# Kernel optimization log

Measured on AMD Instinct MI355X. Metric: run time of the kernel, lower is better.

Reference implementation:

```python
import jax, jax.numpy as jnp
import numpy as np

# ---- Cl(3,0) Cayley table, basis order [1, e1, e2, e3, e12, e13, e23, e123] ----
def _build_cayley():
    order = [0b000, 0b001, 0b010, 0b100, 0b011, 0b101, 0b110, 0b111]
    idx = {m: i for i, m in enumerate(order)}
    M = np.zeros((8, 8, 8), np.float32)
    for i, a in enumerate(order):
        for j, b in enumerate(order):
            aa, swaps = a >> 1, 0
            while aa:
                swaps += bin(aa & b).count('1')
                aa >>= 1
            M[i, j, idx[a ^ b]] = -1.0 if (swaps % 2) else 1.0
    return M

CAYLEY = jnp.asarray(_build_cayley())  # (8,8,8): c_k = a_i b_j M[i,j,k]

B, D, H, R, K = 16384, 512, 256, 95, 8

def _layernorm(x, g, b, eps=1e-5):
    mu = jnp.mean(x, axis=-1, keepdims=True)
    var = jnp.var(x, axis=-1, keepdims=True)
    return (x - mu) * jax.lax.rsqrt(var + eps) * g + b

def _proj(h, W1, b1, lg, lb, W2, b2):
    x = h @ W1 + b1
    x = _layernorm(x, lg, lb)
    x = jax.nn.gelu(x, approximate=False)  # torch nn.GELU default = exact erf
    return (x @ W2 + b2).reshape(h.shape[0], K, 8)  # dropout is eval-mode identity

def setup_inputs() -> dict:
    key = jax.random.key(0)
    ks = jax.random.split(key, 16)
    s1, s2 = 1.0 / np.sqrt(D), 1.0 / np.sqrt(H)
    inp = {
        'h_perp': jax.random.normal(ks[0], (B, D), jnp.float32),
        'h_vuln': jax.random.normal(ks[1], (B, D), jnp.float32),
        'Wp1': jax.random.normal(ks[2], (D, H), jnp.float32) * s1,
        'bp1': jnp.zeros((H,), jnp.float32),
        'lgp': jnp.ones((H,), jnp.float32),
        'lbp': jnp.zeros((H,), jnp.float32),
        'Wp2': jax.random.normal(ks[3], (H, K * 8), jnp.float32) * s2,
        'bp2': jnp.zeros((K * 8,), jnp.float32),
        'Wv1': jax.random.normal(ks[4], (D, H), jnp.float32) * s1,
        'bv1': jnp.zeros((H,), jnp.float32),
        'lgv': jnp.ones((H,), jnp.float32),
        'lbv': jnp.zeros((H,), jnp.float32),
        'Wv2': jax.random.normal(ks[5], (H, K * 8), jnp.float32) * s2,
        'bv2': jnp.zeros((K * 8,), jnp.float32),
        'T': jax.random.normal(ks[6], (R, K, 8), jnp.float32) * 0.1,
        'gw': jnp.zeros((8,), jnp.float32).at[0].set(1.0),
    }
    return inp

def reference(h_perp, h_vuln, Wp1, bp1, lgp, lbp, Wp2, bp2,
              Wv1, bv1, lgv, lbv, Wv2, bv2, T, gw):
    m_perp = _proj(h_perp, Wp1, bp1, lgp, lbp, Wp2, bp2)  # (B,K,8)
    m_vuln = _proj(h_vuln, Wv1, bv1, lgv, lbv, Wv2, bv2)  # (B,K,8)
    # triple product: (m_perp x T_r) x m_vuln  via Cayley tensor
    at = jnp.einsum('bki,rkj,ijm->brkm', m_perp, T, CAYLEY)          # (B,R,K,8)
    res = jnp.einsum('brkm,bkj,mjn->brkn', at, m_vuln, CAYLEY)       # (B,R,K,8)
    weighted = jnp.einsum('brkn,n->brk', res, gw)                    # grade-weighted readout
    return jnp.mean(weighted, axis=-1)                               # (B,R) logits
```

## Files before the change

kernel.cpp:

```cpp
#include <hip/hip_runtime.h>
#include <math.h>


#define B_ 16384
#define D_ 512
#define H_ 256
#define R_ 95

typedef __attribute__((ext_vector_type(8))) short short8;
typedef __attribute__((ext_vector_type(4))) float f32x4;

#define MFMA(a, b, c) __builtin_amdgcn_mfma_f32_16x16x32_bf16(a, b, c, 0, 0, 0)

__device__ __forceinline__ short f2bf(float x) {
    union { float f; unsigned u; } v; v.f = x;
    unsigned r = v.u + 0x7fffu + ((v.u >> 16) & 1u);
    return (short)(r >> 16);
}
__device__ __forceinline__ float bf2f(short s) {
    union { float f; unsigned u; } v;
    v.u = ((unsigned)(unsigned short)s) << 16;
    return v.f;
}

__device__ __forceinline__ float gelu_fast(float x) {
    const float z  = x * 0.70710678118654752f;
    const float az = fabsf(z);
    const float t  = 1.0f / fmaf(0.3275911f, az, 1.0f);
    float p = fmaf(1.061405429f, t, -1.453152027f);
    p = fmaf(p, t, 1.421413741f);
    p = fmaf(p, t, -0.284496736f);
    p = fmaf(p, t, 0.254829592f);
    p *= t;
    const float e  = 1.0f - p * __expf(-az * az);
    const float er = copysignf(e, z);
    return 0.5f * x * (1.0f + er);
}

__global__ __launch_bounds__(256)
void cdd_prep_kernel(const float* __restrict__ Wp1, const float* __restrict__ Wv1,
                     const float* __restrict__ Wp2, const float* __restrict__ Wv2,
                     short* __restrict__ W1c_p, short* __restrict__ W1c_v,
                     short* __restrict__ W2t_p, short* __restrict__ W2t_v)
{
    const int o = blockIdx.x * 256 + threadIdx.x;
    if (o < 16 * 256 * 32) {
        const int n = o & 255, kin = (o >> 8) & 31, ch = o >> 13;
        const int src = (ch * 32 + kin) * 256 + n;
        const int dst = ch * 8192 + n * 32 + kin;
        W1c_p[dst] = f2bf(Wp1[src]);
        W1c_v[dst] = f2bf(Wv1[src]);
    }
    if (o < 64 * 256) {
        const int n = o >> 8, k = o & 255;
        W2t_p[o] = f2bf(Wp2[k * 64 + n]);
        W2t_v[o] = f2bf(Wv2[k * 64 + n]);
    }
}

#define PROJ_BODY(Kk, BUF_C, BUF_R, S_I0, S_I1, S_C0, S_C1, WB_USE, WB_LD)  \
  do {                                                                      \
    const int g = gb + (Kk);                                                \
    if (g <= 14) {                         \
      short8 pk;                                                            \
      pk[0]=f2bf(S_C0.x); pk[1]=f2bf(S_C0.y); pk[2]=f2bf(S_C0.z); pk[3]=f2bf(S_C0.w); \
      pk[4]=f2bf(S_C1.x); pk[5]=f2bf(S_C1.y); pk[6]=f2bf(S_C1.z); pk[7]=f2bf(S_C1.w); \
      *(short8*)(hs + (BUF_C) * 2048 + wdst) = pk;                          \
    }                                                                       \
    asm volatile("s_waitcnt lgkmcnt(0)" ::: "memory");  \
    __builtin_amdgcn_s_barrier();                                           \
    asm volatile("" ::: "memory");                                          \
    if (g <= 14) {                            \
      _Pragma("unroll")                                                     \
      for (int nt = 0; nt < 4; ++nt)                                        \
        WB_LD[nt] = *(const short8*)(Wb0 + (g + 1) * 8192 + nt * 512);      \
    }                                                                       \
    {                                                  \
      const short8 a0 = *(const short8*)(hs + (BUF_R) * 2048 + (0 * 64 + l) * 8); \
      const short8 a1 = *(const short8*)(hs + (BUF_R) * 2048 + (1 * 64 + l) * 8); \
      const short8 a2 = *(const short8*)(hs + (BUF_R) * 2048 + (2 * 64 + l) * 8); \
      const short8 a3 = *(const short8*)(hs + (BUF_R) * 2048 + (3 * 64 + l) * 8); \
      _Pragma("unroll")                                                     \
      for (int nt = 0; nt < 4; ++nt) {                                      \
        acc1[0][nt] = MFMA(a0, WB_USE[nt], acc1[0][nt]);                    \
        acc1[1][nt] = MFMA(a1, WB_USE[nt], acc1[1][nt]);                    \
        acc1[2][nt] = MFMA(a2, WB_USE[nt], acc1[2][nt]);                    \
        acc1[3][nt] = MFMA(a3, WB_USE[nt], acc1[3][nt]);                    \
      }                                                                     \
    }                                                                       \
    asm volatile("" ::: "memory");         \
    if (g <= 11) {                       \
      S_I0 = *(const float4*)(hbase + (g + 4) * 32);                        \
      S_I1 = *(const float4*)(hbase + (g + 4) * 32 + 4);                    \
    }                                                                       \
  } while (0)

__global__ __launch_bounds__(256, 2)
void cdd_proj_kernel(const float* __restrict__ h_p, const float* __restrict__ h_v,
                     const float* __restrict__ bp1, const float* __restrict__ lgp,
                     const float* __restrict__ lbp, const float* __restrict__ bp2,
                     const float* __restrict__ bv1, const float* __restrict__ lgv,
                     const float* __restrict__ lbv, const float* __restrict__ bv2,
                     const short* __restrict__ W1c_p, const short* __restrict__ W1c_v,
                     const short* __restrict__ W2t_p, const short* __restrict__ W2t_v,
                     short* __restrict__ mp_out, short* __restrict__ mv_out)
{
    __shared__ __align__(16) short hs[4 * 2048];
    __shared__ __align__(16) short xs[64 * 264];
    __shared__ __align__(16) float lnbuf[512];

    const int which = blockIdx.y;
    const float* __restrict__ h   = which ? h_v : h_p;
    const float* __restrict__ b1  = which ? bv1 : bp1;
    const float* __restrict__ lg  = which ? lgv : lgp;
    const float* __restrict__ lb  = which ? lbv : lbp;
    const float* __restrict__ b2  = which ? bv2 : bp2;
    const short* __restrict__ W1c = which ? W1c_v : W1c_p;
    const short* __restrict__ W2t = which ? W2t_v : W2t_p;
    short* __restrict__ mo = which ? mv_out : mp_out;

    const int t = threadIdx.x;
    const int w = t >> 6, l = t & 63, q = l >> 4, c = l & 15;
    const int b0 = blockIdx.x * 64;
    const int srow = t >> 2, kq4 = (t & 3);
    const int mt_s = srow >> 4, c_s = srow & 15;
    const int wdst = (mt_s * 64 + kq4 * 16 + c_s) * 8;

    f32x4 acc1[4][4];
#pragma unroll
    for (int mt = 0; mt < 4; ++mt)
#pragma unroll
        for (int nt = 0; nt < 4; ++nt) acc1[mt][nt] = 0;

    const short* Wb0 = W1c + (w * 64 + c) * 32 + q * 8;
    const float* hbase = h + (size_t)(b0 + srow) * D_ + kq4 * 8;

    float4 s0a = *(const float4*)(hbase + 0 * 32), s0b = *(const float4*)(hbase + 0 * 32 + 4);
    float4 s1a = *(const float4*)(hbase + 1 * 32), s1b = *(const float4*)(hbase + 1 * 32 + 4);
    float4 s2a = *(const float4*)(hbase + 2 * 32), s2b = *(const float4*)(hbase + 2 * 32 + 4);
    float4 s3a = *(const float4*)(hbase + 3 * 32), s3b = *(const float4*)(hbase + 3 * 32 + 4);
    short8 wbA[4], wbB[4];
#pragma unroll
    for (int nt = 0; nt < 4; ++nt) wbA[nt] = *(const short8*)(Wb0 + nt * 512);
    {
        short8 pk;
        pk[0]=f2bf(s0a.x); pk[1]=f2bf(s0a.y); pk[2]=f2bf(s0a.z); pk[3]=f2bf(s0a.w);
        pk[4]=f2bf(s0b.x); pk[5]=f2bf(s0b.y); pk[6]=f2bf(s0b.z); pk[7]=f2bf(s0b.w);
        *(short8*)(hs + 0 * 2048 + wdst) = pk;
    }

    for (int gb = 0; gb < 16; gb += 4) {
        PROJ_BODY(0, 1, 0, s0a, s0b, s1a, s1b, wbA, wbB);
        PROJ_BODY(1, 2, 1, s1a, s1b, s2a, s2b, wbB, wbA);
        PROJ_BODY(2, 3, 2, s2a, s2b, s3a, s3b, wbA, wbB);
        PROJ_BODY(3, 0, 3, s3a, s3b, s0a, s0b, wbB, wbA);
    }

    float bb[4], gg[4], ee[4];
#pragma unroll
    for (int nt = 0; nt < 4; ++nt) {
        const int col = w * 64 + nt * 16 + c;
        bb[nt] = b1[col]; gg[nt] = lg[col]; ee[nt] = lb[col];
    }
#pragma unroll
    for (int mt = 0; mt < 4; ++mt)
#pragma unroll
        for (int reg = 0; reg < 4; ++reg) {
            float s1 = 0.f, s2 = 0.f;
#pragma unroll
            for (int nt = 0; nt < 4; ++nt) {
                const float a = acc1[mt][nt][reg] + bb[nt];
                acc1[mt][nt][reg] = a;
                s1 += a; s2 += a * a;
            }
#pragma unroll
            for (int m = 1; m <= 8; m <<= 1) {
                s1 += __shfl_xor(s1, m, 64);
                s2 += __shfl_xor(s2, m, 64);
            }
            if (c == 0) {
                const int row = mt * 16 + q * 4 + reg;
                *(float2*)(lnbuf + (w * 64 + row) * 2) = make_float2(s1, s2);
            }
        }
    __syncthreads();
#pragma unroll
    for (int mt = 0; mt < 4; ++mt)
#pragma unroll
        for (int reg = 0; reg < 4; ++reg) {
            const int row = mt * 16 + q * 4 + reg;
            float S1 = 0.f, S2 = 0.f;
#pragma unroll
            for (int w2 = 0; w2 < 4; ++w2) {
                const float2 p = *(const float2*)(lnbuf + (w2 * 64 + row) * 2);
                S1 += p.x; S2 += p.y;
            }
            const float mu  = S1 * (1.f / 256.f);
            const float var = S2 * (1.f / 256.f) - mu * mu;
            const float rs  = rsqrtf(var + 1e-5f);
#pragma unroll
            for (int nt = 0; nt < 4; ++nt) {
                const int col = w * 64 + nt * 16 + c;
                const float xv = (acc1[mt][nt][reg] - mu) * rs * gg[nt] + ee[nt];
                xs[row * 264 + col] = f2bf(gelu_fast(xv));
            }
        }
    __syncthreads();

    f32x4 acc2[4];
#pragma unroll
    for (int mt = 0; mt < 4; ++mt) acc2[mt] = 0;
    const short* W2b = W2t + (w * 16 + c) * 256 + q * 8;
#pragma unroll
    for (int ks = 0; ks < 8; ++ks) {
        const short8 wbk = *(const short8*)(W2b + ks * 32);
#pragma unroll
        for (int mt = 0; mt < 4; ++mt) {
            const short8 xa = *(const short8*)(xs + (mt * 16 + c) * 264 + ks * 32 + q * 8);
            acc2[mt] = MFMA(xa, wbk, acc2[mt]);
        }
    }
    const float bc = b2[w * 16 + c];
#pragma unroll
    for (int mt = 0; mt < 4; ++mt)
#pragma unroll
        for (int reg = 0; reg < 4; ++reg) {
            const int row = mt * 16 + q * 4 + reg;
            mo[(size_t)(b0 + row) * 64 + w * 16 + c] = f2bf(acc2[mt][reg] + bc);
        }
}

__global__ __launch_bounds__(256, 2)
void cdd_cliff_kernel(const short* __restrict__ mp, const short* __restrict__ mv,
                      const float* __restrict__ T, const float* __restrict__ gw,
                      float* __restrict__ out)
{
    __shared__ __align__(16) float wfl[32 * 68];
    __shared__ __align__(16) float ts[95 * 68];
    const int t  = threadIdx.x;
    const int b0 = blockIdx.x * 32;

#pragma unroll
    for (int k = 0; k < 6; ++k) {
        const int o = t + k * 256;
        if (o < 95 * 16) {
            const int rr = o >> 4, c4 = (o & 15) << 2;
            *(float4*)(ts + rr * 68 + c4) = *(const float4*)(T + rr * 64 + c4);
        }
    }

    {
        const int row = t >> 3, kq = t & 7;
        float g[8];
#pragma unroll
        for (int i = 0; i < 8; ++i) g[i] = gw[i];
        const short8 p8 = *(const short8*)(mp + (size_t)(b0 + row) * 64 + kq * 8);
        const short8 q8 = *(const short8*)(mv + (size_t)(b0 + row) * 64 + kq * 8);
        float mpv[8], mvv[8];
#pragma unroll
        for (int i = 0; i < 8; ++i) { mpv[i] = bf2f(p8[i]); mvv[i] = bf2f(q8[i]); }

        constexpr int MSK[8] = {0, 1, 2, 4, 3, 5, 6, 7};
        float v[8];
#pragma unroll
        for (int m = 0; m < 8; ++m) {
            float s = 0.f;
#pragma unroll
            for (int j = 0; j < 8; ++j) {
                const int am = MSK[m], bm = MSK[j];
                const int par = (__popc((am >> 1) & bm) + __popc((am >> 2) & bm)) & 1;
                const float sg = par ? -1.f : 1.f;
                s = fmaf(sg * g[MSK[am ^ bm]], mvv[j], s);
            }
            v[m] = s;
        }
#pragma unroll
        for (int l2 = 0; l2 < 8; ++l2) {
            float s = 0.f;
#pragma unroll
            for (int i = 0; i < 8; ++i) {
                const int am = MSK[i], bm = MSK[l2];
                const int par = (__popc((am >> 1) & bm) + __popc((am >> 2) & bm)) & 1;
                const float sg = par ? -1.f : 1.f;
                s = fmaf(sg * mpv[i], v[MSK[am ^ bm]], s);
            }
            wfl[row * 68 + kq * 8 + l2] = s;
        }
    }
    __syncthreads();

    {
        const int rr = t >> 3, rl = t & 7;
        float4 wv[16];
#pragma unroll
        for (int cc = 0; cc < 16; ++cc)
            wv[cc] = *(const float4*)(wfl + rr * 68 + cc * 4);
#pragma unroll
        for (int k = 0; k < 12; ++k) {
            const int r = rl + (k << 3);
            if (r < R_) {
                float s = 0.f;
#pragma unroll
                for (int cc = 0; cc < 16; ++cc) {
                    const float4 tv = *(const float4*)(ts + r * 68 + cc * 4);
                    s += wv[cc].x * tv.x + wv[cc].y * tv.y
                       + wv[cc].z * tv.z + wv[cc].w * tv.w;
                }
                out[(size_t)(b0 + rr) * R_ + r] = 0.125f * s;
            }
        }
    }
}

extern "C" void kernel_launch(void* const* d_in, const int* in_sizes, int n_in,
                              void* d_out, int out_size, void* d_ws, size_t ws_size,
                              hipStream_t stream)
{
    const float* h_p = (const float*)d_in[0];
    const float* h_v = (const float*)d_in[1];
    const float* Wp1 = (const float*)d_in[2];
    const float* bp1 = (const float*)d_in[3];
    const float* lgp = (const float*)d_in[4];
    const float* lbp = (const float*)d_in[5];
    const float* Wp2 = (const float*)d_in[6];
    const float* bp2 = (const float*)d_in[7];
    const float* Wv1 = (const float*)d_in[8];
    const float* bv1 = (const float*)d_in[9];
    const float* lgv = (const float*)d_in[10];
    const float* lbv = (const float*)d_in[11];
    const float* Wv2 = (const float*)d_in[12];
    const float* bv2 = (const float*)d_in[13];
    const float* T   = (const float*)d_in[14];
    const float* gw  = (const float*)d_in[15];
    float* out = (float*)d_out;

    short* W1c_p = (short*)d_ws;
    short* W1c_v = W1c_p + 16 * 256 * 32;
    short* W2t_p = W1c_v + 16 * 256 * 32;
    short* W2t_v = W2t_p + 64 * 256;
    short* mp    = W2t_v + 64 * 256;
    short* mv    = mp + (size_t)B_ * 64;

    cdd_prep_kernel<<<512, 256, 0, stream>>>(Wp1, Wv1, Wp2, Wv2,
                                             W1c_p, W1c_v, W2t_p, W2t_v);
    dim3 g1(B_ / 64, 2);
    cdd_proj_kernel<<<g1, 256, 0, stream>>>(h_p, h_v,
                                            bp1, lgp, lbp, bp2,
                                            bv1, lgv, lbv, bv2,
                                            W1c_p, W1c_v, W2t_p, W2t_v,
                                            mp, mv);
    cdd_cliff_kernel<<<B_ / 32, 256, 0, stream>>>(mp, mv, T, gw, out);
}
```

Measured before the change: 155.9 us.

## Fuse projection and Clifford product into one kernel with 32-row tiles

Merges the projection kernel and the Clifford triple-product kernel into a single kernel. Each 32-row block computes both projections sequentially and keeps the resulting multivectors in shared memory instead of writing them to global memory and reading them back. The K loop is restructured to process two 32-wide chunks per barrier, halving the number of barriers and widening the weight double buffer. Risks include higher register and LDS use lowering occupancy, halved M-tile reuse of the weights, and the two projections now running serially within a block.

```diff
diff --git a/kernel.cpp b/kernel.cpp
--- a/kernel.cpp
+++ b/kernel.cpp
@@ -58,187 +58,73 @@
     }
 }
 
-#define PROJ_BODY(Kk, BUF_C, BUF_R, S_I0, S_I1, S_C0, S_C1, WB_USE, WB_LD)  \
-  do {                                                                      \
-    const int g = gb + (Kk);                                                \
-    if (g <= 14) {                         \
-      short8 pk;                                                            \
-      pk[0]=f2bf(S_C0.x); pk[1]=f2bf(S_C0.y); pk[2]=f2bf(S_C0.z); pk[3]=f2bf(S_C0.w); \
-      pk[4]=f2bf(S_C1.x); pk[5]=f2bf(S_C1.y); pk[6]=f2bf(S_C1.z); pk[7]=f2bf(S_C1.w); \
-      *(short8*)(hs + (BUF_C) * 2048 + wdst) = pk;                          \
-    }                                                                       \
-    asm volatile("s_waitcnt lgkmcnt(0)" ::: "memory");  \
-    __builtin_amdgcn_s_barrier();                                           \
-    asm volatile("" ::: "memory");                                          \
-    if (g <= 14) {                            \
-      _Pragma("unroll")                                                     \
-      for (int nt = 0; nt < 4; ++nt)                                        \
-        WB_LD[nt] = *(const short8*)(Wb0 + (g + 1) * 8192 + nt * 512);      \
-    }                                                                       \
-    {                                                  \
-      const short8 a0 = *(const short8*)(hs + (BUF_R) * 2048 + (0 * 64 + l) * 8); \
-      const short8 a1 = *(const short8*)(hs + (BUF_R) * 2048 + (1 * 64 + l) * 8); \
-      const short8 a2 = *(const short8*)(hs + (BUF_R) * 2048 + (2 * 64 + l) * 8); \
-      const short8 a3 = *(const short8*)(hs + (BUF_R) * 2048 + (3 * 64 + l) * 8); \
-      _Pragma("unroll")                                                     \
-      for (int nt = 0; nt < 4; ++nt) {                                      \
-        acc1[0][nt] = MFMA(a0, WB_USE[nt], acc1[0][nt]);                    \
-        acc1[1][nt] = MFMA(a1, WB_USE[nt], acc1[1][nt]);                    \
-        acc1[2][nt] = MFMA(a2, WB_USE[nt], acc1[2][nt]);                    \
-        acc1[3][nt] = MFMA(a3, WB_USE[nt], acc1[3][nt]);                    \
-      }                                                                     \
-    }                                                                       \
-    asm volatile("" ::: "memory");         \
-    if (g <= 11) {                       \
-      S_I0 = *(const float4*)(hbase + (g + 4) * 32);                        \
-      S_I1 = *(const float4*)(hbase + (g + 4) * 32 + 4);                    \
-    }                                                                       \
+#define FBODY(G, BUFC, BUFR, SC_A, SC_B, SI_A, SI_B, WUSE, WLD)              \
+  do {                                                                       \
+    if ((G) <= 6) {                          \
+      short8 pk;                                                             \
+      pk[0]=f2bf(SC_A.x); pk[1]=f2bf(SC_A.y); pk[2]=f2bf(SC_A.z); pk[3]=f2bf(SC_A.w); \
+      pk[4]=f2bf(SC_B.x); pk[5]=f2bf(SC_B.y); pk[6]=f2bf(SC_B.z); pk[7]=f2bf(SC_B.w); \
+      *(short8*)(hs + (BUFC) * 2048 + wdst) = pk;                            \
+    }                                                                        \
+    asm volatile("s_waitcnt lgkmcnt(0)" ::: "memory");   \
+    __builtin_amdgcn_s_barrier();                                            \
+    asm volatile("" ::: "memory");                                           \
+    if ((G) <= 6) {                             \
+      _Pragma("unroll")                                                      \
+      for (int nt = 0; nt < 4; ++nt) {                                       \
+        WLD[nt]     = *(const short8*)(Wb0 + (2*(G)+2) * 8192 + nt * 512);   \
+        WLD[4 + nt] = *(const short8*)(Wb0 + (2*(G)+3) * 8192 + nt * 512);   \
+      }                                                                      \
+    }                                                                        \
+    {                                   \
+      const short8 a00 = *(const short8*)(hs + (BUFR)*2048 + (0*64 + l)*8);  \
+      const short8 a01 = *(const short8*)(hs + (BUFR)*2048 + (1*64 + l)*8);  \
+      const short8 a10 = *(const short8*)(hs + (BUFR)*2048 + (2*64 + l)*8);  \
+      const short8 a11 = *(const short8*)(hs + (BUFR)*2048 + (3*64 + l)*8);  \
+      _Pragma("unroll")                                                      \
+      for (int nt = 0; nt < 4; ++nt) {                                       \
+        acc1[0][nt] = MFMA(a00, WUSE[nt], acc1[0][nt]);                      \
+        acc1[1][nt] = MFMA(a01, WUSE[nt], acc1[1][nt]);                      \
+      }                                                                      \
+      _Pragma("unroll")                                                      \
+      for (int nt = 0; nt < 4; ++nt) {                                       \
+        acc1[0][nt] = MFMA(a10, WUSE[4+nt], acc1[0][nt]);                    \
+        acc1[1][nt] = MFMA(a11, WUSE[4+nt], acc1[1][nt]);                    \
+      }                                                                      \
+    }                                                                        \
+    asm volatile("" ::: "memory");          \
+    if ((G) <= 4) {                        \
+      SI_A = *(const float4*)(hbase + ((G)+3) * 64);                         \
+      SI_B = *(const float4*)(hbase + ((G)+3) * 64 + 4);                     \
+    }                                                                        \
   } while (0)
 
 __global__ __launch_bounds__(256, 2)
-void cdd_proj_kernel(const float* __restrict__ h_p, const float* __restrict__ h_v,
-                     const float* __restrict__ bp1, const float* __restrict__ lgp,
-                     const float* __restrict__ lbp, const float* __restrict__ bp2,
-                     const float* __restrict__ bv1, const float* __restrict__ lgv,
-                     const float* __restrict__ lbv, const float* __restrict__ bv2,
-                     const short* __restrict__ W1c_p, const short* __restrict__ W1c_v,
-                     const short* __restrict__ W2t_p, const short* __restrict__ W2t_v,
-                     short* __restrict__ mp_out, short* __restrict__ mv_out)
-{
-    __shared__ __align__(16) short hs[4 * 2048];
-    __shared__ __align__(16) short xs[64 * 264];
-    __shared__ __align__(16) float lnbuf[512];
-
-    const int which = blockIdx.y;
-    const float* __restrict__ h   = which ? h_v : h_p;
-    const float* __restrict__ b1  = which ? bv1 : bp1;
-    const float* __restrict__ lg  = which ? lgv : lgp;
-    const float* __restrict__ lb  = which ? lbv : lbp;
-    const float* __restrict__ b2  = which ? bv2 : bp2;
-    const short* __restrict__ W1c = which ? W1c_v : W1c_p;
-    const short* __restrict__ W2t = which ? W2t_v : W2t_p;
-    short* __restrict__ mo = which ? mv_out : mp_out;
-
-    const int t = threadIdx.x;
-    const int w = t >> 6, l = t & 63, q = l >> 4, c = l & 15;
-    const int b0 = blockIdx.x * 64;
-    const int srow = t >> 2, kq4 = (t & 3);
-    const int mt_s = srow >> 4, c_s = srow & 15;
-    const int wdst = (mt_s * 64 + kq4 * 16 + c_s) * 8;
-
-    f32x4 acc1[4][4];
-#pragma unroll
-    for (int mt = 0; mt < 4; ++mt)
-#pragma unroll
-        for (int nt = 0; nt < 4; ++nt) acc1[mt][nt] = 0;
-
-    const short* Wb0 = W1c + (w * 64 + c) * 32 + q * 8;
-    const float* hbase = h + (size_t)(b0 + srow) * D_ + kq4 * 8;
-
-    float4 s0a = *(const float4*)(hbase + 0 * 32), s0b = *(const float4*)(hbase + 0 * 32 + 4);
-    float4 s1a = *(const float4*)(hbase + 1 * 32), s1b = *(const float4*)(hbase + 1 * 32 + 4);
-    float4 s2a = *(const float4*)(hbase + 2 * 32), s2b = *(const float4*)(hbase + 2 * 32 + 4);
-    float4 s3a = *(const float4*)(hbase + 3 * 32), s3b = *(const float4*)(hbase + 3 * 32 + 4);
-    short8 wbA[4], wbB[4];
-#pragma unroll
-    for (int nt = 0; nt < 4; ++nt) wbA[nt] = *(const short8*)(Wb0 + nt * 512);
-    {
-        short8 pk;
-        pk[0]=f2bf(s0a.x); pk[1]=f2bf(s0a.y); pk[2]=f2bf(s0a.z); pk[3]=f2bf(s0a.w);
-        pk[4]=f2bf(s0b.x); pk[5]=f2bf(s0b.y); pk[6]=f2bf(s0b.z); pk[7]=f2bf(s0b.w);
-        *(short8*)(hs + 0 * 2048 + wdst) = pk;
-    }
-
-    for (int gb = 0; gb < 16; gb += 4) {
-        PROJ_BODY(0, 1, 0, s0a, s0b, s1a, s1b, wbA, wbB);
-        PROJ_BODY(1, 2, 1, s1a, s1b, s2a, s2b, wbB, wbA);
-        PROJ_BODY(2, 3, 2, s2a, s2b, s3a, s3b, wbA, wbB);
-        PROJ_BODY(3, 0, 3, s3a, s3b, s0a, s0b, wbB, wbA);
-    }
-
-    float bb[4], gg[4], ee[4];
-#pragma unroll
-    for (int nt = 0; nt < 4; ++nt) {
-        const int col = w * 64 + nt * 16 + c;
-        bb[nt] = b1[col]; gg[nt] = lg[col]; ee[nt] = lb[col];
-    }
-#pragma unroll
-    for (int mt = 0; mt < 4; ++mt)
-#pragma unroll
-        for (int reg = 0; reg < 4; ++reg) {
-            float s1 = 0.f, s2 = 0.f;
-#pragma unroll
-            for (int nt = 0; nt < 4; ++nt) {
-                const float a = acc1[mt][nt][reg] + bb[nt];
-                acc1[mt][nt][reg] = a;
-                s1 += a; s2 += a * a;
-            }
-#pragma unroll
-            for (int m = 1; m <= 8; m <<= 1) {
-                s1 += __shfl_xor(s1, m, 64);
-                s2 += __shfl_xor(s2, m, 64);
-            }
-            if (c == 0) {
-                const int row = mt * 16 + q * 4 + reg;
-                *(float2*)(lnbuf + (w * 64 + row) * 2) = make_float2(s1, s2);
-            }
-        }
-    __syncthreads();
-#pragma unroll
-    for (int mt = 0; mt < 4; ++mt)
-#pragma unroll
-        for (int reg = 0; reg < 4; ++reg) {
-            const int row = mt * 16 + q * 4 + reg;
-            float S1 = 0.f, S2 = 0.f;
-#pragma unroll
-            for (int w2 = 0; w2 < 4; ++w2) {
-                const float2 p = *(const float2*)(lnbuf + (w2 * 64 + row) * 2);
-                S1 += p.x; S2 += p.y;
-            }
-            const float mu  = S1 * (1.f / 256.f);
-            const float var = S2 * (1.f / 256.f) - mu * mu;
-            const float rs  = rsqrtf(var + 1e-5f);
-#pragma unroll
-            for (int nt = 0; nt < 4; ++nt) {
-                const int col = w * 64 + nt * 16 + c;
-                const float xv = (acc1[mt][nt][reg] - mu) * rs * gg[nt] + ee[nt];
-                xs[row * 264 + col] = f2bf(gelu_fast(xv));
-            }
-        }
-    __syncthreads();
-
-    f32x4 acc2[4];
-#pragma unroll
-    for (int mt = 0; mt < 4; ++mt) acc2[mt] = 0;
-    const short* W2b = W2t + (w * 16 + c) * 256 + q * 8;
-#pragma unroll
-    for (int ks = 0; ks < 8; ++ks) {
-        const short8 wbk = *(const short8*)(W2b + ks * 32);
-#pragma unroll
-        for (int mt = 0; mt < 4; ++mt) {
-            const short8 xa = *(const short8*)(xs + (mt * 16 + c) * 264 + ks * 32 + q * 8);
-            acc2[mt] = MFMA(xa, wbk, acc2[mt]);
-        }
-    }
-    const float bc = b2[w * 16 + c];
-#pragma unroll
-    for (int mt = 0; mt < 4; ++mt)
-#pragma unroll
-        for (int reg = 0; reg < 4; ++reg) {
-            const int row = mt * 16 + q * 4 + reg;
-            mo[(size_t)(b0 + row) * 64 + w * 16 + c] = f2bf(acc2[mt][reg] + bc);
-        }
-}
-
-__global__ __launch_bounds__(256, 2)
-void cdd_cliff_kernel(const short* __restrict__ mp, const short* __restrict__ mv,
+void cdd_fused_kernel(const float* __restrict__ h_p, const float* __restrict__ h_v,
+                      const float* __restrict__ bp1, const float* __restrict__ lgp,
+                      const float* __restrict__ lbp, const float* __restrict__ bp2,
+                      const float* __restrict__ bv1, const float* __restrict__ lgv,
+                      const float* __restrict__ lbv, const float* __restrict__ bv2,
+                      const short* __restrict__ W1c_p, const short* __restrict__ W1c_v,
+                      const short* __restrict__ W2t_p, const short* __restrict__ W2t_v,
                       const float* __restrict__ T, const float* __restrict__ gw,
                       float* __restrict__ out)
 {
+    __shared__ __align__(16) short hs[4 * 2048];
+    __shared__ __align__(16) short xs[32 * 264];
+    __shared__ __align__(16) float lnbuf[256];
+    __shared__ __align__(16) short mbuf[2 * 2048];
+    __shared__ __align__(16) float ts[95 * 68];
     __shared__ __align__(16) float wfl[32 * 68];
-    __shared__ __align__(16) float ts[95 * 68];
-    const int t  = threadIdx.x;
+
+    const int t = threadIdx.x;
+    const int w = t >> 6, l = t & 63, q = l >> 4, c = l & 15;
     const int b0 = blockIdx.x * 32;
+
+    const int srow = t >> 3, kq8 = t & 7;
+    const int mt_s = srow >> 4, c_s = srow & 15;
+    const int ch_s = kq8 >> 2, q_s = kq8 & 3;
+    const int wdst = ((ch_s * 2 + mt_s) * 64 + q_s * 16 + c_s) * 8;
 
 #pragma unroll
     for (int k = 0; k < 6; ++k) {
@@ -249,13 +135,132 @@
         }
     }
 
+    for (int which = 0; which < 2; ++which) {
+        const float* __restrict__ h   = which ? h_v : h_p;
+        const float* __restrict__ b1  = which ? bv1 : bp1;
+        const float* __restrict__ lg  = which ? lgv : lgp;
+        const float* __restrict__ lb  = which ? lbv : lbp;
+        const float* __restrict__ b2  = which ? bv2 : bp2;
+        const short* __restrict__ W1c = which ? W1c_v : W1c_p;
+        const short* __restrict__ W2t = which ? W2t_v : W2t_p;
+        short* mb = mbuf + which * 2048;
+
+        f32x4 acc1[2][4];
+#pragma unroll
+        for (int mt = 0; mt < 2; ++mt)
+#pragma unroll
+            for (int nt = 0; nt < 4; ++nt) acc1[mt][nt] = 0;
+
+        const short* Wb0 = W1c + (w * 64 + c) * 32 + q * 8;
+        const float* hbase = h + (size_t)(b0 + srow) * D_ + kq8 * 8;
+
+        float4 s0a = *(const float4*)(hbase + 0 * 64), s0b = *(const float4*)(hbase + 0 * 64 + 4);
+        float4 s1a = *(const float4*)(hbase + 1 * 64), s1b = *(const float4*)(hbase + 1 * 64 + 4);
+        float4 s2a = *(const float4*)(hbase + 2 * 64), s2b = *(const float4*)(hbase + 2 * 64 + 4);
+        short8 wbA[8], wbB[8];
+#pragma unroll
+        for (int nt = 0; nt < 4; ++nt) {
+            wbA[nt]     = *(const short8*)(Wb0 + 0 * 8192 + nt * 512);
+            wbA[4 + nt] = *(const short8*)(Wb0 + 1 * 8192 + nt * 512);
+        }
+        {
+            short8 pk;
+            pk[0]=f2bf(s0a.x); pk[1]=f2bf(s0a.y); pk[2]=f2bf(s0a.z); pk[3]=f2bf(s0a.w);
+            pk[4]=f2bf(s0b.x); pk[5]=f2bf(s0b.y); pk[6]=f2bf(s0b.z); pk[7]=f2bf(s0b.w);
+            *(short8*)(hs + 0 * 2048 + wdst) = pk;
+        }
+
+        FBODY(0, 1, 0, s1a, s1b, s0a, s0b, wbA, wbB);
+        FBODY(1, 2, 1, s2a, s2b, s1a, s1b, wbB, wbA);
+        FBODY(2, 3, 2, s0a, s0b, s2a, s2b, wbA, wbB);
+        FBODY(3, 0, 3, s1a, s1b, s0a, s0b, wbB, wbA);
+        FBODY(4, 1, 0, s2a, s2b, s1a, s1b, wbA, wbB);
+        FBODY(5, 2, 1, s0a, s0b, s2a, s2b, wbB, wbA);
+        FBODY(6, 3, 2, s1a, s1b, s0a, s0b, wbA, wbB);
+        FBODY(7, 0, 3, s2a, s2b, s0a, s0b, wbB, wbA);
+
+        float bb[4], gg[4], ee[4];
+#pragma unroll
+        for (int nt = 0; nt < 4; ++nt) {
+            const int col = w * 64 + nt * 16 + c;
+            bb[nt] = b1[col]; gg[nt] = lg[col]; ee[nt] = lb[col];
+        }
+#pragma unroll
+        for (int mt = 0; mt < 2; ++mt)
+#pragma unroll
+            for (int reg = 0; reg < 4; ++reg) {
+                float s1 = 0.f, s2 = 0.f;
+#pragma unroll
+                for (int nt = 0; nt < 4; ++nt) {
+                    const float a = acc1[mt][nt][reg] + bb[nt];
+                    acc1[mt][nt][reg] = a;
+                    s1 += a; s2 += a * a;
+                }
+#pragma unroll
+                for (int m = 1; m <= 8; m <<= 1) {
+                    s1 += __shfl_xor(s1, m, 64);
+                    s2 += __shfl_xor(s2, m, 64);
+                }
+                if (c == 0) {
+                    const int row = mt * 16 + q * 4 + reg;
+                    *(float2*)(lnbuf + (w * 32 + row) * 2) = make_float2(s1, s2);
+                }
+            }
+        __syncthreads();
+#pragma unroll
+        for (int mt = 0; mt < 2; ++mt)
+#pragma unroll
+            for (int reg = 0; reg < 4; ++reg) {
+                const int row = mt * 16 + q * 4 + reg;
+                float S1 = 0.f, S2 = 0.f;
+#pragma unroll
+                for (int w2 = 0; w2 < 4; ++w2) {
+                    const float2 p = *(const float2*)(lnbuf + (w2 * 32 + row) * 2);
+                    S1 += p.x; S2 += p.y;
+                }
+                const float mu  = S1 * (1.f / 256.f);
+                const float var = S2 * (1.f / 256.f) - mu * mu;
+                const float rs  = rsqrtf(var + 1e-5f);
+#pragma unroll
+                for (int nt = 0; nt < 4; ++nt) {
+                    const int col = w * 64 + nt * 16 + c;
+                    const float xv = (acc1[mt][nt][reg] - mu) * rs * gg[nt] + ee[nt];
+                    xs[row * 264 + col] = f2bf(gelu_fast(xv));
+                }
+            }
+        __syncthreads();
+
+        f32x4 acc2[2];
+#pragma unroll
+        for (int mt2 = 0; mt2 < 2; ++mt2) acc2[mt2] = 0;
+        const short* W2b = W2t + (w * 16 + c) * 256 + q * 8;
+#pragma unroll
+        for (int ks = 0; ks < 8; ++ks) {
+            const short8 wbk = *(const short8*)(W2b + ks * 32);
+#pragma unroll
+            for (int mt2 = 0; mt2 < 2; ++mt2) {
+                const short8 xa = *(const short8*)(xs + (mt2 * 16 + c) * 264 + ks * 32 + q * 8);
+                acc2[mt2] = MFMA(xa, wbk, acc2[mt2]);
+            }
+        }
+        const float bc = b2[w * 16 + c];
+#pragma unroll
+        for (int mt2 = 0; mt2 < 2; ++mt2)
+#pragma unroll
+            for (int reg = 0; reg < 4; ++reg) {
+                const int row = mt2 * 16 + q * 4 + reg;
+                mb[row * 64 + w * 16 + c] = f2bf(acc2[mt2][reg] + bc);
+            }
+        __syncthreads();
+    }
+
     {
         const int row = t >> 3, kq = t & 7;
         float g[8];
 #pragma unroll
         for (int i = 0; i < 8; ++i) g[i] = gw[i];
-        const short8 p8 = *(const short8*)(mp + (size_t)(b0 + row) * 64 + kq * 8);
-        const short8 q8 = *(const short8*)(mv + (size_t)(b0 + row) * 64 + kq * 8);
+        const short8 p8 = *(const short8*)(mbuf + row * 64 + kq * 8);
+        const short8 q8 = *(const short8*)(mbuf + 2048 + row * 64 + kq * 8);
         float mpv[8], mvv[8];
 #pragma unroll
         for (int i = 0; i < 8; ++i) { mpv[i] = bf2f(p8[i]); mvv[i] = bf2f(q8[i]); }
@@ -338,16 +343,12 @@
     short* W1c_v = W1c_p + 16 * 256 * 32;
     short* W2t_p = W1c_v + 16 * 256 * 32;
     short* W2t_v = W2t_p + 64 * 256;
-    short* mp    = W2t_v + 64 * 256;
-    short* mv    = mp + (size_t)B_ * 64;
 
     cdd_prep_kernel<<<512, 256, 0, stream>>>(Wp1, Wv1, Wp2, Wv2,
                                              W1c_p, W1c_v, W2t_p, W2t_v);
-    dim3 g1(B_ / 64, 2);
-    cdd_proj_kernel<<<g1, 256, 0, stream>>>(h_p, h_v,
-                                            bp1, lgp, lbp, bp2,
-                                            bv1, lgv, lbv, bv2,
-                                            W1c_p, W1c_v, W2t_p, W2t_v,
-                                            mp, mv);
-    cdd_cliff_kernel<<<B_ / 32, 256, 0, stream>>>(mp, mv, T, gw, out);
-}
+    cdd_fused_kernel<<<B_ / 32, 256, 0, stream>>>(h_p, h_v,
+                                                  bp1, lgp, lbp, bp2,
+                                                  bv1, lgv, lbv, bv2,
+                                                  W1c_p, W1c_v, W2t_p, W2t_v,
+                                                  T, gw, out);
+}
```

New measurement: 156.4 us. No clear change (+0.4%).
